# Optimization experiments

Measured on AMD Instinct MI355X. Metric: run time of the kernel, lower is better.

The kernel has to match this reference:

```python
import jax, jax.numpy as jnp
import numpy as np

HG, WG, DG = 16, 16, 8   # bilateral grid size
NP = 12                  # affine params per pixel (3x4)
DS = 256                 # input_downsample


def _resize_bilinear(x, oh, ow):
    # torch F.interpolate(mode='bilinear', align_corners=False)
    B, C, H, W = x.shape
    sy, sx = H / oh, W / ow
    ys = jnp.clip((jnp.arange(oh, dtype=x.dtype) + 0.5) * sy - 0.5, 0.0, H - 1)
    xs = jnp.clip((jnp.arange(ow, dtype=x.dtype) + 0.5) * sx - 0.5, 0.0, W - 1)
    y0 = jnp.floor(ys).astype(jnp.int32); y1 = jnp.minimum(y0 + 1, H - 1)
    x0 = jnp.floor(xs).astype(jnp.int32); x1 = jnp.minimum(x0 + 1, W - 1)
    wy = (ys - y0.astype(x.dtype))[None, None, :, None]
    wx = (xs - x0.astype(x.dtype))[None, None, None, :]
    top = x[:, :, y0, :] * (1 - wy) + x[:, :, y1, :] * wy      # [B,C,oh,W]
    return top[:, :, :, x0] * (1 - wx) + top[:, :, :, x1] * wx  # [B,C,oh,ow]


def _conv(x, w, b):
    y = jax.lax.conv_general_dilated(x, w, (1, 1), 'SAME',
                                     dimension_numbers=('NCHW', 'OIHW', 'NCHW'))
    return y + b[None, :, None, None]


def _slice(grid, guide):
    # grid [B,C,Hg,Wg,D], guide [B,H,W] in [0,1].
    # Equivalent to the per-depth grid_sample(align_corners=True, border) +
    # depth gather/lerp loop: one fused trilinear lookup per pixel.
    B, C, Hg, Wg, D = grid.shape
    H, W = guide.shape[1], guide.shape[2]
    ys = jnp.arange(H, dtype=grid.dtype) * ((Hg - 1) / (H - 1))
    xs = jnp.arange(W, dtype=grid.dtype) * ((Wg - 1) / (W - 1))
    y0 = jnp.floor(ys).astype(jnp.int32); y1 = jnp.minimum(y0 + 1, Hg - 1)
    x0 = jnp.floor(xs).astype(jnp.int32); x1 = jnp.minimum(x0 + 1, Wg - 1)
    wy = (ys - y0.astype(grid.dtype))[:, None]   # [H,1]
    wx = (xs - x0.astype(grid.dtype))[None, :]   # [1,W]
    d = guide * (D - 1)
    d0 = jnp.clip(jnp.floor(d), 0, D - 1).astype(jnp.int32)
    d1 = jnp.minimum(d0 + 1, D - 1)
    wd = jnp.clip(d - d0.astype(grid.dtype), 0.0, 1.0)  # [B,H,W]

    Y0, Y1 = y0[:, None], y1[:, None]
    X0, X1 = x0[None, :], x1[None, :]

    def per_b(g, d0b, d1b, wdb):
        def dlerp(yi, xi):
            # g[:, yi, xi, d] -> [C,H,W]; lerp over depth
            return (1 - wdb) * g[:, yi, xi, d0b] + wdb * g[:, yi, xi, d1b]
        return ((1 - wy) * (1 - wx) * dlerp(Y0, X0)
                + (1 - wy) * wx * dlerp(Y0, X1)
                + wy * (1 - wx) * dlerp(Y1, X0)
                + wy * wx * dlerp(Y1, X1))

    return jax.vmap(per_b)(grid, d0, d1, wd)  # [B,C,H,W]


def _forward(x, w1, b1, w2, b2, w3, b3, w4, b4, w5, b5, w6, b6):
    B, C, H, W = x.shape
    guide = jnp.clip(0.299 * x[:, 0] + 0.587 * x[:, 1] + 0.114 * x[:, 2], 0.0, 1.0)
    scale = min(1.0, DS / max(H, W))
    if scale < 1.0:
        x_low = _resize_bilinear(x, int(H * scale), int(W * scale))
    else:
        x_low = x
    f = jax.nn.relu(_conv(x_low, w1, b1))
    f = jax.nn.relu(_conv(f, w2, b2))
    f = jax.nn.relu(_conv(f, w3, b3))
    c = jax.nn.relu(_conv(f, w4, b4))
    c = jax.nn.relu(_conv(c, w5, b5))
    c = _conv(c, w6, b6)                        # [B, NP*DG, H_low, W_low]
    c = _resize_bilinear(c, HG, WG)             # [B, NP*DG, HG, WG]
    grid = c.reshape(B, NP, DG, HG, WG).transpose(0, 1, 3, 4, 2)  # [B,NP,HG,WG,DG]
    sc = _slice(grid, guide)                    # [B, NP, H, W]
    co = sc.reshape(B, 3, 4, H, W)
    y = jnp.einsum('bijhw,bjhw->bihw', co[:, :, :3], x) + co[:, :, 3]
    return jnp.clip(y, 0.0, 1.0)


def setup_inputs() -> dict:
    key = jax.random.key(0)
    ks = jax.random.split(key, 7)
    x = jax.random.uniform(ks[0], (2, 3, 1024, 1024), dtype=jnp.float32)
    def wmat(k, o, i):
        return jax.random.normal(k, (o, i, 3, 3), jnp.float32) / np.sqrt(i * 9.0)
    return dict(
        x=x,
        w1=wmat(ks[1], 16, 3), b1=jnp.zeros((16,), jnp.float32),
        w2=wmat(ks[2], 32, 16), b2=jnp.zeros((32,), jnp.float32),
        w3=wmat(ks[3], 32, 32), b3=jnp.zeros((32,), jnp.float32),
        w4=wmat(ks[4], 64, 32), b4=jnp.zeros((64,), jnp.float32),
        w5=wmat(ks[5], 64, 64), b5=jnp.zeros((64,), jnp.float32),
        w6=wmat(ks[6], 96, 64), b6=jnp.zeros((96,), jnp.float32),
    )


def reference(x, w1, b1, w2, b2, w3, b3, w4, b4, w5, b5, w6, b6):
    return _forward(x, w1, b1, w2, b2, w3, b3, w4, b4, w5, b5, w6, b6)
```

## Files before the change

### kernel.cpp

```cpp
#include <hip/hip_runtime.h>
#include <hip/hip_bf16.h>

#define HW1K  1048576

typedef float  f4    __attribute__((ext_vector_type(4)));
typedef float  f32x4 __attribute__((ext_vector_type(4)));
typedef short  s16x8 __attribute__((ext_vector_type(8)));
typedef unsigned short u16x8 __attribute__((ext_vector_type(8)));

__device__ __forceinline__ float bf2f(unsigned short u) {
    unsigned int b = ((unsigned int)u) << 16;
    return __builtin_bit_cast(float, b);
}
__device__ __forceinline__ void fsplit(float x, unsigned short& h, unsigned short& l) {
    unsigned int xb = __builtin_bit_cast(unsigned int, x);
    h = (unsigned short)(xb >> 16);
    float fh = __builtin_bit_cast(float, xb & 0xffff0000u);
    float r = x - fh;
    l = (unsigned short)(__builtin_bit_cast(unsigned int, r) >> 16);
}

__global__ __launch_bounds__(256)
void prep_wM(const float* __restrict__ w2, const float* __restrict__ w3,
             const float* __restrict__ w4, const float* __restrict__ w5,
             const float* __restrict__ w6,
             unsigned short* __restrict__ Wh, unsigned short* __restrict__ Wl) {
    int i = blockIdx.x * 256 + threadIdx.x;
    if (i >= 124928) return;
    const float* src; int base, cin, kp_;
    if      (i < 5120)  { src = w2; base = 0;     cin = 16; kp_ = 160; }
    else if (i < 14336) { src = w3; base = 5120;  cin = 32; kp_ = 288; }
    else if (i < 32768) { src = w4; base = 14336; cin = 32; kp_ = 288; }
    else if (i < 69632) { src = w5; base = 32768; cin = 64; kp_ = 576; }
    else                { src = w6; base = 69632; cin = 64; kp_ = 576; }
    int r  = i - base;
    int co = r / kp_;
    int kp = r % kp_;
    int kk = kp / cin;
    int ci = kp % cin;
    float v = (kk < 9) ? src[(co * cin + ci) * 9 + kk] : 0.0f;
    unsigned short h, l; fsplit(v, h, l);
    Wh[i] = h; Wl[i] = l;
}

template <int WIN, int CIN, int COUT, int KP, int SO>
__device__ __forceinline__ void layerM(const unsigned short* sH, const unsigned short* sL,
                                       unsigned short* dH, unsigned short* dL,
                                       const unsigned short* __restrict__ Wh,
                                       const unsigned short* __restrict__ Wl,
                                       const float* __restrict__ bias) {
    constexpr int WOUT = WIN - 2;
    constexpr int NPX  = WOUT * WOUT;
    constexpr int CINP = CIN + 8;
    constexpr int MT   = (NPX + 15) / 16;
    constexpr int NT   = COUT / 16;
    constexpr int PAIRS = MT * NT;

    const int wid  = threadIdx.x >> 6;
    const int lane = threadIdx.x & 63;
    const int m    = lane & 15;
    const int g    = lane >> 4;

    #pragma unroll 1
    for (int p = wid; p < PAIRS; p += 4) {
        const int mt0 = (p / NT) * 16;
        const int nt0 = (p % NT) * 16;
        int px = mt0 + m; if (px > NPX - 1) px = NPX - 1;
        const int pbase = (px / WOUT) * WIN + (px % WOUT);
        const int co = nt0 + m;
        const unsigned short* wbh = Wh + (size_t)co * KP + 8 * g;
        const unsigned short* wbl = Wl + (size_t)co * KP + 8 * g;

        f32x4 aHH = {0,0,0,0}, aHL = {0,0,0,0}, aLH = {0,0,0,0};
        for (int k0 = 0; k0 < KP; k0 += 32) {
            const int k   = k0 + 8 * g;
            const int kk  = k / CIN;
            const int ci0 = k % CIN;
            const int aoff = (pbase + (kk / 3) * WIN + (kk % 3)) * CINP + ci0;
            s16x8 avh = *(const s16x8*)(&sH[aoff]);
            s16x8 avl = *(const s16x8*)(&sL[aoff]);
            s16x8 bvh = *(const s16x8*)(wbh + k0);
            s16x8 bvl = *(const s16x8*)(wbl + k0);
            aHH = __builtin_amdgcn_mfma_f32_16x16x32_bf16(avh, bvh, aHH, 0, 0, 0);
            aHL = __builtin_amdgcn_mfma_f32_16x16x32_bf16(avh, bvl, aHL, 0, 0, 0);
            aLH = __builtin_amdgcn_mfma_f32_16x16x32_bf16(avl, bvh, aLH, 0, 0, 0);
        }
        const float bv = bias[co];
        #pragma unroll
        for (int j = 0; j < 4; ++j) {
            int opx = mt0 + g * 4 + j;
            if (opx < NPX) {
                float v = aHH[j] + aHL[j] + aLH[j] + bv;
                v = fmaxf(v, 0.0f);
                unsigned short h, l; fsplit(v, h, l);
                dH[opx * SO + co] = h;
                dL[opx * SO + co] = l;
            }
        }
    }
}

__global__ __launch_bounds__(256)
void fusedM(const float* __restrict__ x, const float* __restrict__ w1,
            const float* __restrict__ b1,
            const unsigned short* __restrict__ Wh, const unsigned short* __restrict__ Wl,
            const float* __restrict__ b2, const float* __restrict__ b3,
            const float* __restrict__ b4, const float* __restrict__ b5,
            unsigned short* __restrict__ A5h, unsigned short* __restrict__ A5l) {
    __shared__ float sC[592];
    __shared__ __align__(16) unsigned short AH[3840], AL[3840];
    __shared__ __align__(16) unsigned short BH[4000], BL[4000];

    const int cell = blockIdx.x;
    const int b = cell >> 8, gy = (cell >> 4) & 15, gx = cell & 15;

    for (int i = threadIdx.x; i < 588; i += 256) {
        int c = i / 196, t = i % 196;
        int xi = t % 14, yi = t / 14;
        int ya = 16 * gy + 1 + yi, xa = 16 * gx + 1 + xi;
        const float* p = x + ((size_t)(b * 3 + c)) * HW1K + (4 * ya + 1) * 1024 + (4 * xa + 1);
        sC[i] = 0.25f * (p[0] + p[1] + p[1024] + p[1025]);
    }
    for (int i = threadIdx.x; i < 384; i += 256) { AH[3456 + i] = 0; AL[3456 + i] = 0; }
    __syncthreads();

    {
        const int wid  = __builtin_amdgcn_readfirstlane(threadIdx.x >> 6);
        const int lane = threadIdx.x & 63;
        const int co0  = wid * 4;
        float acc[3][4]; int pxs[3], pb[3];
        #pragma unroll
        for (int t = 0; t < 3; ++t) {
            int px = lane + t * 64; if (px > 143) px = 143;
            pxs[t] = px; pb[t] = (px / 12) * 14 + (px % 12);
            #pragma unroll
            for (int j = 0; j < 4; ++j) acc[t][j] = b1[co0 + j];
        }
        for (int ci = 0; ci < 3; ++ci)
            #pragma unroll
            for (int k = 0; k < 9; ++k) {
                float w[4];
                #pragma unroll
                for (int j = 0; j < 4; ++j) w[j] = w1[((co0 + j) * 3 + ci) * 9 + k];
                const int ko = (k / 3) * 14 + (k % 3);
                #pragma unroll
                for (int t = 0; t < 3; ++t) {
                    float a = sC[ci * 196 + pb[t] + ko];
                    #pragma unroll
                    for (int j = 0; j < 4; ++j) acc[t][j] = fmaf(w[j], a, acc[t][j]);
                }
            }
        #pragma unroll
        for (int t = 0; t < 3; ++t)
            #pragma unroll
            for (int j = 0; j < 4; ++j) {
                float v = fmaxf(acc[t][j], 0.0f);
                unsigned short h, l; fsplit(v, h, l);
                AH[pxs[t] * 24 + co0 + j] = h;
                AL[pxs[t] * 24 + co0 + j] = l;
            }
    }
    __syncthreads();

    layerM<12, 16, 32, 160, 40>(AH, AL, BH, BL, Wh + 0,     Wl + 0,     b2);
    __syncthreads();
    layerM<10, 32, 32, 288, 40>(BH, BL, AH, AL, Wh + 5120,  Wl + 5120,  b3);
    __syncthreads();
    layerM< 8, 32, 64, 288, 72>(AH, AL, BH, BL, Wh + 14336, Wl + 14336, b4);
    __syncthreads();
    layerM< 6, 64, 64, 576, 64>(BH, BL, A5h + (size_t)cell * 1024, A5l + (size_t)cell * 1024,
                                Wh + 32768, Wl + 32768, b5);
}

__global__ __launch_bounds__(256)
void pool5(const unsigned short* __restrict__ A5h, const unsigned short* __restrict__ A5l,
           unsigned short* __restrict__ Bh, unsigned short* __restrict__ Bl) {
    int idx = blockIdx.x * 256 + threadIdx.x;
    if (idx >= 512 * 576) return;
    int cell = idx / 576, kp = idx % 576;
    int kk = kp >> 6, ci = kp & 63;
    int ky = kk / 3, kx = kk % 3;
    float v = 0.0f;
    #pragma unroll
    for (int dr = 0; dr < 2; ++dr)
        #pragma unroll
        for (int dc = 0; dc < 2; ++dc) {
            int px = (ky + dr) * 4 + (kx + dc);
            size_t ai = ((size_t)cell * 16 + px) * 64 + ci;
            v += bf2f(A5h[ai]) + bf2f(A5l[ai]);
        }
    v *= 0.25f;
    unsigned short h, l; fsplit(v, h, l);
    Bh[idx] = h; Bl[idx] = l;
}

__global__ __launch_bounds__(64)
void gemm6(const unsigned short* __restrict__ Bh, const unsigned short* __restrict__ Bl,
           const unsigned short* __restrict__ W6h, const unsigned short* __restrict__ W6l,
           const float* __restrict__ b6, float* __restrict__ c16) {
    const int cell0 = blockIdx.x * 16;
    const int co0   = blockIdx.y * 16;
    const int lane  = threadIdx.x;
    const int m = lane & 15, g = lane >> 4;

    const unsigned short* pah = Bh  + (size_t)(cell0 + m) * 576 + 8 * g;
    const unsigned short* pal = Bl  + (size_t)(cell0 + m) * 576 + 8 * g;
    const unsigned short* pbh = W6h + (size_t)(co0 + m) * 576 + 8 * g;
    const unsigned short* pbl = W6l + (size_t)(co0 + m) * 576 + 8 * g;

    f32x4 aHH = {0,0,0,0}, aHL = {0,0,0,0}, aLH = {0,0,0,0};
    for (int k0 = 0; k0 < 576; k0 += 32) {
        s16x8 avh = *(const s16x8*)(pah + k0);
        s16x8 avl = *(const s16x8*)(pal + k0);
        s16x8 bvh = *(const s16x8*)(pbh + k0);
        s16x8 bvl = *(const s16x8*)(pbl + k0);
        aHH = __builtin_amdgcn_mfma_f32_16x16x32_bf16(avh, bvh, aHH, 0, 0, 0);
        aHL = __builtin_amdgcn_mfma_f32_16x16x32_bf16(avh, bvl, aHL, 0, 0, 0);
        aLH = __builtin_amdgcn_mfma_f32_16x16x32_bf16(avl, bvh, aLH, 0, 0, 0);
    }
    const int co = co0 + m;
    const float bv = b6[co];
    #pragma unroll
    for (int j = 0; j < 4; ++j) {
        int cell = cell0 + g * 4 + j;
        float v = aHH[j] + aHL[j] + aLH[j] + bv;
        int b = cell >> 8, gyx = cell & 255;
        c16[(size_t)b * 24576 + (gyx * 8 + (co & 7)) * 12 + (co >> 3)] = v;
    }
}

__global__ __launch_bounds__(256)
void slice_apply4(const float* __restrict__ x, const float* __restrict__ c16,
                  float* __restrict__ out) {
    int t = blockIdx.x * 256 + threadIdx.x;
    int po4 = t * 4;
    int b   = po4 >> 20;
    int po  = po4 & (HW1K - 1);
    int py  = po >> 10;
    int px0 = po & 1023;

    const float* xb = x + (size_t)b * 3 * HW1K;
    f4 rv  = *(const f4*)(xb + po);
    f4 gv  = *(const f4*)(xb + HW1K + po);
    f4 bv  = *(const f4*)(xb + 2 * HW1K + po);

    float ysf = (float)py * (15.0f / 1023.0f);
    int y0 = (int)floorf(ysf); int y1 = min(y0 + 1, 15);
    float wy = ysf - (float)y0;

    const float* gb = c16 + (size_t)b * 24576;
    f4 outv[3];

    #pragma unroll
    for (int s = 0; s < 4; ++s) {
        float r  = rv[s], g = gv[s], bl = bv[s];
        int   px = px0 + s;

        float gd = fminf(fmaxf(0.299f * r + 0.587f * g + 0.114f * bl, 0.0f), 1.0f);

        float xsf = (float)px * (15.0f / 1023.0f);
        int x0 = (int)floorf(xsf); int x1 = min(x0 + 1, 15);
        float wx = xsf - (float)x0;

        float d  = gd * 7.0f;
        int d0 = (int)floorf(d); d0 = max(0, min(d0, 7));
        int d1 = min(d0 + 1, 7);
        float wd = fminf(fmaxf(d - (float)d0, 0.0f), 1.0f);

        float co[12];
        #pragma unroll
        for (int p = 0; p < 12; ++p) co[p] = 0.0f;

        #pragma unroll
        for (int cy = 0; cy < 2; ++cy) {
            int   yy  = cy ? y1 : y0;
            float wyf = cy ? wy : 1.0f - wy;
            #pragma unroll
            for (int cx = 0; cx < 2; ++cx) {
                int   xx  = cx ? x1 : x0;
                float wyx = wyf * (cx ? wx : 1.0f - wx);
                const float* g0 = gb + ((yy * 16 + xx) * 8 + d0) * 12;
                const float* g1 = gb + ((yy * 16 + xx) * 8 + d1) * 12;
                float wA = wyx * (1.0f - wd), wB = wyx * wd;
                #pragma unroll
                for (int p = 0; p < 12; ++p) co[p] += wA * g0[p] + wB * g1[p];
            }
        }

        #pragma unroll
        for (int i = 0; i < 3; ++i) {
            float v = co[i * 4 + 0] * r + co[i * 4 + 1] * g + co[i * 4 + 2] * bl + co[i * 4 + 3];
            outv[i][s] = fminf(fmaxf(v, 0.0f), 1.0f);
        }
    }

    float* ob = out + (size_t)b * 3 * HW1K;
    #pragma unroll
    for (int i = 0; i < 3; ++i)
        *(f4*)(ob + i * HW1K + po) = outv[i];
}

extern "C" void kernel_launch(void* const* d_in, const int* in_sizes, int n_in,
                              void* d_out, int out_size, void* d_ws, size_t ws_size,
                              hipStream_t stream) {
    const float* x  = (const float*)d_in[0];
    const float* w1 = (const float*)d_in[1];  const float* b1 = (const float*)d_in[2];
    const float* w2 = (const float*)d_in[3];  const float* b2 = (const float*)d_in[4];
    const float* w3 = (const float*)d_in[5];  const float* b3 = (const float*)d_in[6];
    const float* w4 = (const float*)d_in[7];  const float* b4 = (const float*)d_in[8];
    const float* w5 = (const float*)d_in[9];  const float* b5 = (const float*)d_in[10];
    const float* w6 = (const float*)d_in[11]; const float* b6 = (const float*)d_in[12];
    float* out = (float*)d_out;

    char* w = (char*)d_ws;
    unsigned short* Wh  = (unsigned short*)w;   w += 124928 * 2;
    unsigned short* Wl  = (unsigned short*)w;   w += 124928 * 2;
    unsigned short* A5h = (unsigned short*)w;   w += 512 * 1024 * 2;
    unsigned short* A5l = (unsigned short*)w;   w += 512 * 1024 * 2;
    unsigned short* P6h = (unsigned short*)w;   w += 512 * 576 * 2;
    unsigned short* P6l = (unsigned short*)w;   w += 512 * 576 * 2;
    float*          c16 = (float*)w;

    prep_wM<<<dim3(489),  dim3(256), 0, stream>>>(w2, w3, w4, w5, w6, Wh, Wl);
    fusedM <<<dim3(512),  dim3(256), 0, stream>>>(x, w1, b1, Wh, Wl, b2, b3, b4, b5, A5h, A5l);
    pool5  <<<dim3(1152), dim3(256), 0, stream>>>(A5h, A5l, P6h, P6l);
    gemm6  <<<dim3(32, 6), dim3(64), 0, stream>>>(P6h, P6l, Wh + 69632, Wl + 69632, b6, c16);
    slice_apply4<<<dim3(2 * HW1K / 4 / 256), dim3(256), 0, stream>>>(x, c16, out);

    (void)in_sizes; (void)n_in; (void)out_size; (void)ws_size;
}
```

Measured before the change: 75.36 us.

## Fuse pool into conv stack and keep layer weights in registers

The separate pool5 kernel is folded into fusedM: layer 5 now writes to shared memory and each block average-pools its own cell before storing P6, which removes one launch and the A5 global round trip. layerM assigns each wave a fixed output-channel tile and preloads all its weight fragments into registers once, so only activation loads remain in the inner loop. It also adds launch_bounds occupancy 2 and an unroll hint in gemm6. Holding the full weight arrays in registers (up to 36 s16x8 for layer 5) raises register pressure, which may cause spills under the 2-block bound.

```diff
diff --git a/kernel.cpp b/kernel.cpp
--- a/kernel.cpp
+++ b/kernel.cpp
@@ -54,44 +54,54 @@
     constexpr int CINP = CIN + 8;
     constexpr int MT   = (NPX + 15) / 16;
     constexpr int NT   = COUT / 16;
-    constexpr int PAIRS = MT * NT;
+    constexpr int WPN  = 4 / NT;
+    constexpr int KS   = KP / 32;
 
     const int wid  = threadIdx.x >> 6;
     const int lane = threadIdx.x & 63;
     const int m    = lane & 15;
     const int g    = lane >> 4;
 
+    const int nt    = wid % NT;
+    const int chunk = wid / NT;
+    const int co    = nt * 16 + m;
+
+    s16x8 bH[KS], bL[KS];
+    {
+        const unsigned short* wbh = Wh + (size_t)co * KP + 8 * g;
+        const unsigned short* wbl = Wl + (size_t)co * KP + 8 * g;
+        #pragma unroll
+        for (int k0 = 0; k0 < KS; ++k0) {
+            bH[k0] = *(const s16x8*)(wbh + k0 * 32);
+            bL[k0] = *(const s16x8*)(wbl + k0 * 32);
+        }
+    }
+    const float bv = bias[co];
+
     #pragma unroll 1
-    for (int p = wid; p < PAIRS; p += 4) {
-        const int mt0 = (p / NT) * 16;
-        const int nt0 = (p % NT) * 16;
+    for (int mt = chunk; mt < MT; mt += WPN) {
+        const int mt0 = mt * 16;
         int px = mt0 + m; if (px > NPX - 1) px = NPX - 1;
         const int pbase = (px / WOUT) * WIN + (px % WOUT);
-        const int co = nt0 + m;
-        const unsigned short* wbh = Wh + (size_t)co * KP + 8 * g;
-        const unsigned short* wbl = Wl + (size_t)co * KP + 8 * g;
 
         f32x4 aHH = {0,0,0,0}, aHL = {0,0,0,0}, aLH = {0,0,0,0};
-        for (int k0 = 0; k0 < KP; k0 += 32) {
-            const int k   = k0 + 8 * g;
+        #pragma unroll
+        for (int k0 = 0; k0 < KS; ++k0) {
+            const int k   = k0 * 32 + 8 * g;
             const int kk  = k / CIN;
             const int ci0 = k % CIN;
             const int aoff = (pbase + (kk / 3) * WIN + (kk % 3)) * CINP + ci0;
             s16x8 avh = *(const s16x8*)(&sH[aoff]);
             s16x8 avl = *(const s16x8*)(&sL[aoff]);
-            s16x8 bvh = *(const s16x8*)(wbh + k0);
-            s16x8 bvl = *(const s16x8*)(wbl + k0);
-            aHH = __builtin_amdgcn_mfma_f32_16x16x32_bf16(avh, bvh, aHH, 0, 0, 0);
-            aHL = __builtin_amdgcn_mfma_f32_16x16x32_bf16(avh, bvl, aHL, 0, 0, 0);
-            aLH = __builtin_amdgcn_mfma_f32_16x16x32_bf16(avl, bvh, aLH, 0, 0, 0);
-        }
-        const float bv = bias[co];
+            aHH = __builtin_amdgcn_mfma_f32_16x16x32_bf16(avh, bH[k0], aHH, 0, 0, 0);
+            aHL = __builtin_amdgcn_mfma_f32_16x16x32_bf16(avh, bL[k0], aHL, 0, 0, 0);
+            aLH = __builtin_amdgcn_mfma_f32_16x16x32_bf16(avl, bH[k0], aLH, 0, 0, 0);
+        }
         #pragma unroll
         for (int j = 0; j < 4; ++j) {
             int opx = mt0 + g * 4 + j;
             if (opx < NPX) {
-                float v = aHH[j] + aHL[j] + aLH[j] + bv;
-                v = fmaxf(v, 0.0f);
+                float v = fmaxf(aHH[j] + aHL[j] + aLH[j] + bv, 0.0f);
                 unsigned short h, l; fsplit(v, h, l);
                 dH[opx * SO + co] = h;
                 dL[opx * SO + co] = l;
@@ -100,13 +110,13 @@
     }
 }
 
-__global__ __launch_bounds__(256)
+__global__ __launch_bounds__(256, 2)
 void fusedM(const float* __restrict__ x, const float* __restrict__ w1,
             const float* __restrict__ b1,
             const unsigned short* __restrict__ Wh, const unsigned short* __restrict__ Wl,
             const float* __restrict__ b2, const float* __restrict__ b3,
             const float* __restrict__ b4, const float* __restrict__ b5,
-            unsigned short* __restrict__ A5h, unsigned short* __restrict__ A5l) {
+            unsigned short* __restrict__ P6h, unsigned short* __restrict__ P6l) {
     __shared__ float sC[592];
     __shared__ __align__(16) unsigned short AH[3840], AL[3840];
     __shared__ __align__(16) unsigned short BH[4000], BL[4000];
@@ -168,30 +178,25 @@
     __syncthreads();
     layerM< 8, 32, 64, 288, 72>(AH, AL, BH, BL, Wh + 14336, Wl + 14336, b4);
     __syncthreads();
-    layerM< 6, 64, 64, 576, 64>(BH, BL, A5h + (size_t)cell * 1024, A5l + (size_t)cell * 1024,
-                                Wh + 32768, Wl + 32768, b5);
-}
-
-__global__ __launch_bounds__(256)
-void pool5(const unsigned short* __restrict__ A5h, const unsigned short* __restrict__ A5l,
-           unsigned short* __restrict__ Bh, unsigned short* __restrict__ Bl) {
-    int idx = blockIdx.x * 256 + threadIdx.x;
-    if (idx >= 512 * 576) return;
-    int cell = idx / 576, kp = idx % 576;
-    int kk = kp >> 6, ci = kp & 63;
-    int ky = kk / 3, kx = kk % 3;
-    float v = 0.0f;
-    #pragma unroll
-    for (int dr = 0; dr < 2; ++dr)
-        #pragma unroll
-        for (int dc = 0; dc < 2; ++dc) {
-            int px = (ky + dr) * 4 + (kx + dc);
-            size_t ai = ((size_t)cell * 16 + px) * 64 + ci;
-            v += bf2f(A5h[ai]) + bf2f(A5l[ai]);
-        }
-    v *= 0.25f;
-    unsigned short h, l; fsplit(v, h, l);
-    Bh[idx] = h; Bl[idx] = l;
+    layerM< 6, 64, 64, 576, 72>(BH, BL, AH, AL, Wh + 32768, Wl + 32768, b5);
+    __syncthreads();
+
+    for (int t = threadIdx.x; t < 576; t += 256) {
+        int kk = t >> 6, ci = t & 63;
+        int ky = kk / 3, kx = kk % 3;
+        float v = 0.0f;
+        #pragma unroll
+        for (int dr = 0; dr < 2; ++dr)
+            #pragma unroll
+            for (int dc = 0; dc < 2; ++dc) {
+                int px = (ky + dr) * 4 + (kx + dc);
+                v += bf2f(AH[px * 72 + ci]) + bf2f(AL[px * 72 + ci]);
+            }
+        v *= 0.25f;
+        unsigned short h, l; fsplit(v, h, l);
+        P6h[(size_t)cell * 576 + t] = h;
+        P6l[(size_t)cell * 576 + t] = l;
+    }
 }
 
 __global__ __launch_bounds__(64)
@@ -209,6 +214,7 @@
     const unsigned short* pbl = W6l + (size_t)(co0 + m) * 576 + 8 * g;
 
     f32x4 aHH = {0,0,0,0}, aHL = {0,0,0,0}, aLH = {0,0,0,0};
+    #pragma unroll 6
     for (int k0 = 0; k0 < 576; k0 += 32) {
         s16x8 avh = *(const s16x8*)(pah + k0);
         s16x8 avl = *(const s16x8*)(pal + k0);
@@ -315,15 +321,12 @@
     char* w = (char*)d_ws;
     unsigned short* Wh  = (unsigned short*)w;   w += 124928 * 2;
     unsigned short* Wl  = (unsigned short*)w;   w += 124928 * 2;
-    unsigned short* A5h = (unsigned short*)w;   w += 512 * 1024 * 2;
-    unsigned short* A5l = (unsigned short*)w;   w += 512 * 1024 * 2;
     unsigned short* P6h = (unsigned short*)w;   w += 512 * 576 * 2;
     unsigned short* P6l = (unsigned short*)w;   w += 512 * 576 * 2;
     float*          c16 = (float*)w;
 
     prep_wM<<<dim3(489),  dim3(256), 0, stream>>>(w2, w3, w4, w5, w6, Wh, Wl);
-    fusedM <<<dim3(512),  dim3(256), 0, stream>>>(x, w1, b1, Wh, Wl, b2, b3, b4, b5, A5h, A5l);
-    pool5  <<<dim3(1152), dim3(256), 0, stream>>>(A5h, A5l, P6h, P6l);
+    fusedM <<<dim3(512),  dim3(256), 0, stream>>>(x, w1, b1, Wh, Wl, b2, b3, b4, b5, P6h, P6l);
     gemm6  <<<dim3(32, 6), dim3(64), 0, stream>>>(P6h, P6l, Wh + 69632, Wl + 69632, b6, c16);
     slice_apply4<<<dim3(2 * HW1K / 4 / 256), dim3(256), 0, stream>>>(x, c16, out);
 
```

Result: faster. 66.60 us, median of 3 (-11.6%).
